# Kernel optimization log

Measured on AMD Instinct MI355X. Metric: run time of the kernel, lower is better.

## Reference

```python
import jax, jax.numpy as jnp
import numpy as np

MUL = 64                      # multiplicity of both 0e and 1o irreps
N_NODES = 10000
N_EDGES = 320000
DIM = MUL + 3 * MUL           # 64x0e + 64x1o = 256
SQ3 = float(np.sqrt(3.0))
INV_MUL = float(1.0 / np.sqrt(MUL))        # fan-in norm for irreps Linear
INV_TP = float(1.0 / np.sqrt(2 * MUL))     # fan-in norm: 2 CG paths per output irrep


def _split(f):
    # f: [E_or_N, 256] -> scalars [.,64], vectors [.,64,3]
    return f[:, :MUL], f[:, MUL:].reshape(f.shape[0], MUL, 3)


def _lin(x0, x1, w0, w1):
    # e3nn-style irreps Linear: block-diagonal per l, shared across m
    return (x0 @ w0) * INV_MUL, jnp.einsum('eum,uv->evm', x1, w1) * INV_MUL


def _fctp(x0, x1, sh1, w00, w11, w01, w10):
    # FullyConnectedTensorProduct (64x0e+64x1o) x (1x0e+1x1o) -> (64x0e+64x1o)
    # CG paths: 0e*0e->0e (identity), 1o*1o->0e (dot/sqrt3), 0e*1o->1o, 1o*0e->1o.
    # l=0 spherical harmonic == 1, so 0e SH multiplications are no-ops.
    dot = jnp.einsum('eum,em->eu', x1, sh1) / SQ3
    out0 = (x0 @ w00 + dot @ w11) * INV_TP
    out1 = (jnp.einsum('eu,uv->ev', x0, w01)[:, :, None] * sh1[:, None, :]
            + jnp.einsum('eum,uv->evm', x1, w10)) * INV_TP
    return out0, out1


def _forward(atom_feature, edge_vector, weights, edge_index):
    (ls0, ls1, ld0, ld1,
     t1_00, t1_11, t1_01, t1_10,
     t2_00, t2_11, t2_01, t2_10,
     lh0, lh1, lsc) = weights
    src, dst = edge_index[0], edge_index[1]

    # spherical harmonics of normalized edge vectors (component normalization)
    r = edge_vector / (jnp.linalg.norm(edge_vector, axis=-1, keepdims=True) + 1e-12)
    sh1 = SQ3 * r  # [E,3]; Y_0 == 1 is implicit

    x0, x1 = _split(atom_feature)
    s0, s1 = _lin(x0[src], x1[src], ls0, ls1)
    d0, d1 = _lin(x0[dst], x1[dst], ld0, ld1)  # computed but unused in the original forward

    h0, h1 = _fctp(s0, s1, sh1, t1_00, t1_11, t1_01, t1_10)
    h0, h1 = _lin(h0, h1, lh0, lh1)

    # lin_scalar: Linear(64x0e -> 64x0e+64x1o); only scalar->scalar path exists,
    # vector channels of the output are structurally zero; softmax runs over all 256.
    sc = (jax.nn.leaky_relu(h0) @ lsc) * INV_MUL
    full = jnp.concatenate([sc, jnp.zeros((sc.shape[0], 3 * MUL), sc.dtype)], axis=-1)
    act = jax.nn.softmax(full, axis=-1)  # [E,256]

    o0, o1 = _fctp(h0, h1, sh1, t2_00, t2_11, t2_01, t2_10)
    tp2_flat = jnp.concatenate([o0, o1.reshape(o1.shape[0], 3 * MUL)], axis=-1)

    msgs = act * tp2_flat  # [E,256]
    agg = jax.ops.segment_sum(msgs, dst, num_segments=atom_feature.shape[0])
    return atom_feature + agg  # residual (irreps_in == irreps_out)


_WNAMES = ['lin_src_w0', 'lin_src_w1', 'lin_dst_w0', 'lin_dst_w1',
           'tp1_w00', 'tp1_w11', 'tp1_w01', 'tp1_w10',
           'tp2_w00', 'tp2_w11', 'tp2_w01', 'tp2_w10',
           'lin_hidden_w0', 'lin_hidden_w1', 'lin_scalar_w']


def setup_inputs() -> dict:
    key = jax.random.key(0)
    ks = jax.random.split(key, 18)
    inp = {n: jax.random.normal(ks[i], (MUL, MUL), jnp.float32) for i, n in enumerate(_WNAMES)}
    inp['atom_feature'] = jax.random.normal(ks[15], (N_NODES, DIM), jnp.float32)
    inp['edge_vector'] = jax.random.normal(ks[16], (N_EDGES, 3), jnp.float32)
    inp['edge_index'] = jax.random.randint(ks[17], (2, N_EDGES), 0, N_NODES, dtype=jnp.int32)
    return inp


def reference(atom_feature, edge_vector,
              lin_src_w0, lin_src_w1, lin_dst_w0, lin_dst_w1,
              tp1_w00, tp1_w11, tp1_w01, tp1_w10,
              tp2_w00, tp2_w11, tp2_w01, tp2_w10,
              lin_hidden_w0, lin_hidden_w1, lin_scalar_w,
              edge_index):
    weights = (lin_src_w0, lin_src_w1, lin_dst_w0, lin_dst_w1,
               tp1_w00, tp1_w11, tp1_w01, tp1_w10,
               tp2_w00, tp2_w11, tp2_w01, tp2_w10,
               lin_hidden_w0, lin_hidden_w1, lin_scalar_w)
    return _forward(atom_feature, edge_vector, weights, edge_index)
```

## Files before the change

kernel.cpp:

```cpp
#include <hip/hip_runtime.h>

#define N_NODES 10000
#define N_EDGES 320000
#define DIM 256

typedef __attribute__((ext_vector_type(8))) short bf16x8;
typedef __attribute__((ext_vector_type(4))) float f32x4;

static constexpr float SQ3     = 1.7320508075688772f;
static constexpr float INV_SQ3 = 0.5773502691896258f;
static constexpr float INV_MUL = 0.125f;
static constexpr float INV_TP  = 0.08838834764831845f;

__device__ __forceinline__ unsigned short f2bf(float f) {
    unsigned b = __builtin_bit_cast(unsigned, f);
    b += 0x7FFFu + ((b >> 16) & 1u);
    return (unsigned short)(b >> 16);
}
__device__ __forceinline__ float bf2f(unsigned short h) {
    return __builtin_bit_cast(float, ((unsigned)h) << 16);
}

__device__ __forceinline__ f32x4 MFMA(bf16x8 a, bf16x8 b, f32x4 c) {
    return __builtin_amdgcn_mfma_f32_16x16x32_bf16(a, b, c, 0, 0, 0);
}

struct AF { bf16x8 hi[2], lo[2]; };

__device__ __forceinline__ void split8(const float* v, bf16x8& hi, bf16x8& lo) {
#pragma unroll
    for (int j = 0; j < 8; ++j) {
        unsigned short h = f2bf(v[j]);
        hi[j] = (short)h;
        lo[j] = (short)f2bf(v[j] - bf2f(h));
    }
}

__device__ __forceinline__ void zacc(f32x4* a) {
#pragma unroll
    for (int i = 0; i < 4; ++i) a[i] = (f32x4){0.f, 0.f, 0.f, 0.f};
}

__device__ __forceinline__ void mv_acc(const AF& a, const unsigned short* __restrict__ wm,
                                       f32x4* acc) {
    const int l = threadIdx.x & 63;
#pragma unroll
    for (int ks = 0; ks < 2; ++ks) {
#pragma unroll
        for (int nt = 0; nt < 4; ++nt) {
            bf16x8 bh = *(const bf16x8*)(wm + (ks * 4 + nt) * 512 + l * 8);
            bf16x8 bl = *(const bf16x8*)(wm + 4096 + (ks * 4 + nt) * 512 + l * 8);
            acc[nt] = MFMA(a.hi[ks], bh, acc[nt]);
            acc[nt] = MFMA(a.lo[ks], bh, acc[nt]);
            acc[nt] = MFMA(a.hi[ks], bl, acc[nt]);
        }
    }
}

__device__ __forceinline__ void store_D(float* __restrict__ buf, const f32x4* acc, float scale) {
    const int l = threadIdx.x & 63;
    const int c = l & 15, rgp = l >> 4;
#pragma unroll
    for (int nt = 0; nt < 4; ++nt)
#pragma unroll
        for (int r = 0; r < 4; ++r)
            buf[(rgp * 4 + r) * 68 + nt * 16 + c] = acc[nt][r] * scale;
}

__device__ __forceinline__ void store_D_h1(float* __restrict__ buf, const f32x4* p01,
                                           const float shDm[4], const f32x4* acc) {
    const int l = threadIdx.x & 63;
    const int c = l & 15, rgp = l >> 4;
#pragma unroll
    for (int nt = 0; nt < 4; ++nt)
#pragma unroll
        for (int r = 0; r < 4; ++r)
            buf[(rgp * 4 + r) * 68 + nt * 16 + c] =
                (p01[nt][r] * shDm[r] + acc[nt][r]) * INV_TP;
}

__device__ __forceinline__ void read_row8(const float* __restrict__ buf, int ks, float* v) {
    const int l = threadIdx.x & 63;
    const float* p = buf + (l & 15) * 68 + (l >> 4) * 8 + ks * 32;
    f32x4 x = *(const f32x4*)(p);
    f32x4 y = *(const f32x4*)(p + 4);
    v[0] = x[0]; v[1] = x[1]; v[2] = x[2]; v[3] = x[3];
    v[4] = y[0]; v[5] = y[1]; v[6] = y[2]; v[7] = y[3];
}

__device__ __forceinline__ void build_A(const float* __restrict__ buf, AF& a) {
#pragma unroll
    for (int ks = 0; ks < 2; ++ks) {
        float v[8];
        read_row8(buf, ks, v);
        split8(v, a.hi[ks], a.lo[ks]);
    }
}

__device__ __forceinline__ void build_A_dot(const float* __restrict__ buf, AF& a, float shm,
                                            float dv[2][8]) {
#pragma unroll
    for (int ks = 0; ks < 2; ++ks) {
        float v[8];
        read_row8(buf, ks, v);
#pragma unroll
        for (int j = 0; j < 8; ++j) dv[ks][j] = fmaf(v[j], shm, dv[ks][j]);
        split8(v, a.hi[ks], a.lo[ks]);
    }
}

__device__ __forceinline__ void build_A_leaky(const float* __restrict__ buf, AF& a, AF& alr) {
#pragma unroll
    for (int ks = 0; ks < 2; ++ks) {
        float v[8];
        read_row8(buf, ks, v);
        split8(v, a.hi[ks], a.lo[ks]);
        float w[8];
#pragma unroll
        for (int j = 0; j < 8; ++j) w[j] = v[j] > 0.f ? v[j] : 0.01f * v[j];
        split8(w, alr.hi[ks], alr.lo[ks]);
    }
}

__global__ __launch_bounds__(256) void init_out_kernel(const float* __restrict__ af,
                                                       float* __restrict__ out) {
    int i = blockIdx.x * blockDim.x + threadIdx.x;
    reinterpret_cast<float4*>(out)[i] = reinterpret_cast<const float4*>(af)[i];
}

__global__ __launch_bounds__(256) void prep_w(
    const float* a0, const float* a1, const float* a2, const float* a3,
    const float* a4, const float* a5, const float* a6, const float* a7,
    const float* a8, const float* a9, const float* a10, const float* a11,
    const float* a12, unsigned short* __restrict__ o)
{
    const float* mats[13] = {a0,a1,a2,a3,a4,a5,a6,a7,a8,a9,a10,a11,a12};
    const float* W = mats[blockIdx.x];
    unsigned short* dst = o + blockIdx.x * 8192;
    for (int t = threadIdx.x; t < 4096; t += 256) {
        int u = t >> 6, v = t & 63;
        float val = W[t];
        unsigned short hi = f2bf(val);
        unsigned short lo = f2bf(val - bf2f(hi));
        int ks = u >> 5, g = (u >> 3) & 3, j = u & 7;
        int base = ((ks * 4 + (v >> 4)) * 64 + ((v & 15) + 16 * g)) * 8 + j;
        dst[base] = hi;
        dst[4096 + base] = lo;
    }
}

__global__ __launch_bounds__(256, 2) void edge_kernel(
    const float* __restrict__ af, const float* __restrict__ ev,
    const int* __restrict__ ei, const unsigned short* __restrict__ wb,
    float* __restrict__ out)
{
    __shared__ float lds[4][4][16 * 68];
    const int l  = threadIdx.x & 63;
    const int wv = threadIdx.x >> 6;
    const int rg = l >> 4;
    const int e0 = (blockIdx.x * 4 + wv) * 16;
    float* B0 = lds[wv][0];
    float* B1 = lds[wv][1];
    float* B2 = lds[wv][2];
    float* B3 = lds[wv][3];
    float* Bm[3] = {B1, B2, B3};

    float shA[3];
    {
        int e = e0 + (l & 15);
        float x = ev[3*e], y = ev[3*e+1], z = ev[3*e+2];
        float s = SQ3 / (sqrtf(x*x + y*y + z*z) + 1e-12f);
        shA[0] = x*s; shA[1] = y*s; shA[2] = z*s;
    }
    float shD[4][3]; int dstD[4];
#pragma unroll
    for (int r = 0; r < 4; ++r) {
        int e = e0 + rg * 4 + r;
        float x = ev[3*e], y = ev[3*e+1], z = ev[3*e+2];
        float s = SQ3 / (sqrtf(x*x + y*y + z*z) + 1e-12f);
        shD[r][0] = x*s; shD[r][1] = y*s; shD[r][2] = z*s;
        dstD[r] = ei[N_EDGES + e];
    }

    AF x0a, x1a[3];
    {
        const int node = ei[e0 + (l & 15)];
        const float* rp = af + (long)node * DIM;
#pragma unroll
        for (int ks = 0; ks < 2; ++ks) {
            const int u0 = rg * 8 + ks * 32;
            f32x4 xa = *(const f32x4*)(rp + u0);
            f32x4 xb = *(const f32x4*)(rp + u0 + 4);
            float v[8] = {xa[0],xa[1],xa[2],xa[3],xb[0],xb[1],xb[2],xb[3]};
            split8(v, x0a.hi[ks], x0a.lo[ks]);
            f32x4 sp[6];
#pragma unroll
            for (int q = 0; q < 6; ++q) sp[q] = *(const f32x4*)(rp + 64 + 3 * u0 + 4 * q);
#pragma unroll
            for (int m = 0; m < 3; ++m) {
                float w[8];
#pragma unroll
                for (int j = 0; j < 8; ++j) { int idx = 3 * j + m; w[j] = sp[idx >> 2][idx & 3]; }
                split8(w, x1a[m].hi[ks], x1a[m].lo[ks]);
            }
        }
    }

    f32x4 acc[4];

#pragma unroll
    for (int m = 0; m < 3; ++m) {
        zacc(acc); mv_acc(x1a[m], wb + 1 * 8192, acc);
        store_D(Bm[m], acc, INV_MUL);
    }
    zacc(acc); mv_acc(x0a, wb + 0 * 8192, acc);
    store_D(B0, acc, INV_MUL);
    asm volatile("s_waitcnt lgkmcnt(0)" ::: "memory");

    AF s0a, s1a[3], dota;
    build_A(B0, s0a);
    {
        float dv[2][8] = {};
#pragma unroll
        for (int m = 0; m < 3; ++m) build_A_dot(Bm[m], s1a[m], shA[m], dv);
        float d0[8], d1[8];
#pragma unroll
        for (int j = 0; j < 8; ++j) { d0[j] = dv[0][j] * INV_SQ3; d1[j] = dv[1][j] * INV_SQ3; }
        split8(d0, dota.hi[0], dota.lo[0]);
        split8(d1, dota.hi[1], dota.lo[1]);
    }

    zacc(acc); mv_acc(s0a, wb + 2 * 8192, acc); mv_acc(dota, wb + 3 * 8192, acc);
    store_D(B0, acc, INV_TP);
    f32x4 p01[4];
    zacc(p01); mv_acc(s0a, wb + 4 * 8192, p01);
#pragma unroll
    for (int m = 0; m < 3; ++m) {
        zacc(acc); mv_acc(s1a[m], wb + 5 * 8192, acc);
        float shm[4] = {shD[0][m], shD[1][m], shD[2][m], shD[3][m]};
        store_D_h1(Bm[m], p01, shm, acc);
    }
    asm volatile("s_waitcnt lgkmcnt(0)" ::: "memory");

    AF h0a, h1a[3];
    build_A(B0, h0a);
#pragma unroll
    for (int m = 0; m < 3; ++m) build_A(Bm[m], h1a[m]);
    zacc(acc); mv_acc(h0a, wb + 6 * 8192, acc);
    store_D(B0, acc, INV_MUL);
#pragma unroll
    for (int m = 0; m < 3; ++m) {
        zacc(acc); mv_acc(h1a[m], wb + 7 * 8192, acc);
        store_D(Bm[m], acc, INV_MUL);
    }
    asm volatile("s_waitcnt lgkmcnt(0)" ::: "memory");

    AF g0a, lra, g1a[3], dot2a;
    build_A_leaky(B0, g0a, lra);
    {
        float dv[2][8] = {};
#pragma unroll
        for (int m = 0; m < 3; ++m) build_A_dot(Bm[m], g1a[m], shA[m], dv);
        float d0[8], d1[8];
#pragma unroll
        for (int j = 0; j < 8; ++j) { d0[j] = dv[0][j] * INV_SQ3; d1[j] = dv[1][j] * INV_SQ3; }
        split8(d0, dot2a.hi[0], dot2a.lo[0]);
        split8(d1, dot2a.hi[1], dot2a.lo[1]);
    }

    f32x4 sc[4];
    zacc(sc); mv_acc(lra, wb + 8 * 8192, sc);
    float act1r[4];
    {
#pragma unroll
        for (int nt = 0; nt < 4; ++nt) sc[nt] *= INV_MUL;
#pragma unroll
        for (int r = 0; r < 4; ++r) {
            float mx = fmaxf(fmaxf(sc[0][r], sc[1][r]), fmaxf(sc[2][r], sc[3][r]));
#pragma unroll
            for (int w = 1; w <= 8; w <<= 1) mx = fmaxf(mx, __shfl_xor(mx, w, 64));
            mx = fmaxf(mx, 0.f);
            float s_ = 0.f;
#pragma unroll
            for (int nt = 0; nt < 4; ++nt) { float p = __expf(sc[nt][r] - mx); sc[nt][r] = p; s_ += p; }
#pragma unroll
            for (int w = 1; w <= 8; w <<= 1) s_ += __shfl_xor(s_, w, 64);
            float ez = __expf(-mx);
            float invZ = 1.0f / (s_ + 192.f * ez);
#pragma unroll
            for (int nt = 0; nt < 4; ++nt) sc[nt][r] *= invZ;
            act1r[r] = ez * invZ;
        }
    }

    f32x4 o0[4];
    zacc(o0); mv_acc(g0a, wb + 9 * 8192, o0); mv_acc(dot2a, wb + 10 * 8192, o0);
    f32x4 qD[4];
    zacc(qD); mv_acc(g0a, wb + 11 * 8192, qD);

#pragma unroll
    for (int nt = 0; nt < 4; ++nt)
#pragma unroll
        for (int r = 0; r < 4; ++r)
            atomicAdd(out + (long)dstD[r] * DIM + nt * 16 + (l & 15),
                      sc[nt][r] * o0[nt][r] * INV_TP);

#pragma unroll
    for (int m = 0; m < 3; ++m) {
        zacc(acc); mv_acc(g1a[m], wb + 12 * 8192, acc);
#pragma unroll
        for (int nt = 0; nt < 4; ++nt)
#pragma unroll
            for (int r = 0; r < 4; ++r) {
                float val = (qD[nt][r] * shD[r][m] + acc[nt][r]) * INV_TP * act1r[r];
                atomicAdd(out + (long)dstD[r] * DIM + 64 + 3 * (nt * 16 + (l & 15)) + m, val);
            }
    }
}

extern "C" void kernel_launch(void* const* d_in, const int* in_sizes, int n_in,
                              void* d_out, int out_size, void* d_ws, size_t ws_size,
                              hipStream_t stream) {
    const float* ls0  = (const float*)d_in[0];
    const float* ls1  = (const float*)d_in[1];
    const float* t100 = (const float*)d_in[4];
    const float* t111 = (const float*)d_in[5];
    const float* t101 = (const float*)d_in[6];
    const float* t110 = (const float*)d_in[7];
    const float* t200 = (const float*)d_in[8];
    const float* t211 = (const float*)d_in[9];
    const float* t201 = (const float*)d_in[10];
    const float* t210 = (const float*)d_in[11];
    const float* lh0  = (const float*)d_in[12];
    const float* lh1  = (const float*)d_in[13];
    const float* lsc  = (const float*)d_in[14];
    const float* af   = (const float*)d_in[15];
    const float* ev   = (const float*)d_in[16];
    const int*   ei   = (const int*)d_in[17];
    float* out = (float*)d_out;
    unsigned short* wbuf = (unsigned short*)d_ws;

    hipLaunchKernelGGL(prep_w, dim3(13), dim3(256), 0, stream,
                       ls0, ls1, t100, t111, t101, t110, lh0, lh1, lsc,
                       t200, t211, t201, t210, wbuf);

    hipLaunchKernelGGL(init_out_kernel, dim3(N_NODES * DIM / 4 / 256), dim3(256), 0, stream,
                       af, out);

    hipLaunchKernelGGL(edge_kernel, dim3(N_EDGES / 64), dim3(256), 0, stream,
                       af, ev, ei, wbuf, out);
}
```

Measured before the change: 785.3 us.

## Halve per-wave LDS staging buffers and raise occupancy to four blocks

Each wave's LDS staging shrinks from four 16x68 buffers to two, and the matmul stages are reordered to ping-pong between them. Each build reads a buffer right after its store, with an explicit LDS wait. This cuts LDS per block in half, and launch_bounds is raised from 2 to 4 blocks per CU to use that for more occupancy. The cost is more frequent lgkmcnt waits, which serialise store and read phases, and a tighter register budget that may cause spills.

New measurement: 863.0 us. 9.9% more time.

```diff
diff --git a/kernel.cpp b/kernel.cpp
--- a/kernel.cpp
+++ b/kernel.cpp
@@ -149,21 +149,20 @@
     }
 }
 
-__global__ __launch_bounds__(256, 2) void edge_kernel(
+#define WAIT_LDS asm volatile("s_waitcnt lgkmcnt(0)" ::: "memory")
+
+__global__ __launch_bounds__(256, 4) void edge_kernel(
     const float* __restrict__ af, const float* __restrict__ ev,
     const int* __restrict__ ei, const unsigned short* __restrict__ wb,
     float* __restrict__ out)
 {
-    __shared__ float lds[4][4][16 * 68];
+    __shared__ float lds[4][2][16 * 68];
     const int l  = threadIdx.x & 63;
     const int wv = threadIdx.x >> 6;
     const int rg = l >> 4;
     const int e0 = (blockIdx.x * 4 + wv) * 16;
     float* B0 = lds[wv][0];
     float* B1 = lds[wv][1];
-    float* B2 = lds[wv][2];
-    float* B3 = lds[wv][3];
-    float* Bm[3] = {B1, B2, B3};
 
     float shA[3];
     {
@@ -207,22 +206,18 @@
     }
 
     f32x4 acc[4];
-
-#pragma unroll
-    for (int m = 0; m < 3; ++m) {
-        zacc(acc); mv_acc(x1a[m], wb + 1 * 8192, acc);
-        store_D(Bm[m], acc, INV_MUL);
-    }
-    zacc(acc); mv_acc(x0a, wb + 0 * 8192, acc);
-    store_D(B0, acc, INV_MUL);
-    asm volatile("s_waitcnt lgkmcnt(0)" ::: "memory");
-
     AF s0a, s1a[3], dota;
-    build_A(B0, s0a);
+
+    zacc(acc); mv_acc(x1a[0], wb + 1 * 8192, acc); store_D(B0, acc, INV_MUL);
+    zacc(acc); mv_acc(x1a[1], wb + 1 * 8192, acc); store_D(B1, acc, INV_MUL);
     {
         float dv[2][8] = {};
-#pragma unroll
-        for (int m = 0; m < 3; ++m) build_A_dot(Bm[m], s1a[m], shA[m], dv);
+        WAIT_LDS; build_A_dot(B0, s1a[0], shA[0], dv);
+        zacc(acc); mv_acc(x1a[2], wb + 1 * 8192, acc); store_D(B0, acc, INV_MUL);
+        WAIT_LDS; build_A_dot(B1, s1a[1], shA[1], dv);
+        zacc(acc); mv_acc(x0a, wb + 0 * 8192, acc); store_D(B1, acc, INV_MUL);
+        WAIT_LDS; build_A_dot(B0, s1a[2], shA[2], dv);
+        build_A(B1, s0a);
         float d0[8], d1[8];
 #pragma unroll
         for (int j = 0; j < 8; ++j) { d0[j] = dv[0][j] * INV_SQ3; d1[j] = dv[1][j] * INV_SQ3; }
@@ -230,37 +225,39 @@
         split8(d1, dota.hi[1], dota.lo[1]);
     }
 
+    AF h0a, h1a[3];
     zacc(acc); mv_acc(s0a, wb + 2 * 8192, acc); mv_acc(dota, wb + 3 * 8192, acc);
     store_D(B0, acc, INV_TP);
     f32x4 p01[4];
     zacc(p01); mv_acc(s0a, wb + 4 * 8192, p01);
-#pragma unroll
-    for (int m = 0; m < 3; ++m) {
-        zacc(acc); mv_acc(s1a[m], wb + 5 * 8192, acc);
-        float shm[4] = {shD[0][m], shD[1][m], shD[2][m], shD[3][m]};
-        store_D_h1(Bm[m], p01, shm, acc);
-    }
-    asm volatile("s_waitcnt lgkmcnt(0)" ::: "memory");
-
-    AF h0a, h1a[3];
-    build_A(B0, h0a);
-#pragma unroll
-    for (int m = 0; m < 3; ++m) build_A(Bm[m], h1a[m]);
+    zacc(acc); mv_acc(s1a[0], wb + 5 * 8192, acc);
+    { float shm[4] = {shD[0][0], shD[1][0], shD[2][0], shD[3][0]};
+      store_D_h1(B1, p01, shm, acc); }
+    WAIT_LDS; build_A(B0, h0a);
+    zacc(acc); mv_acc(s1a[1], wb + 5 * 8192, acc);
+    { float shm[4] = {shD[0][1], shD[1][1], shD[2][1], shD[3][1]};
+      store_D_h1(B0, p01, shm, acc); }
+    WAIT_LDS; build_A(B1, h1a[0]);
+    zacc(acc); mv_acc(s1a[2], wb + 5 * 8192, acc);
+    { float shm[4] = {shD[0][2], shD[1][2], shD[2][2], shD[3][2]};
+      store_D_h1(B1, p01, shm, acc); }
+    WAIT_LDS; build_A(B0, h1a[1]);
     zacc(acc); mv_acc(h0a, wb + 6 * 8192, acc);
     store_D(B0, acc, INV_MUL);
-#pragma unroll
-    for (int m = 0; m < 3; ++m) {
-        zacc(acc); mv_acc(h1a[m], wb + 7 * 8192, acc);
-        store_D(Bm[m], acc, INV_MUL);
-    }
-    asm volatile("s_waitcnt lgkmcnt(0)" ::: "memory");
-
+    WAIT_LDS; build_A(B1, h1a[2]);
+    zacc(acc); mv_acc(h1a[0], wb + 7 * 8192, acc);
+    store_D(B1, acc, INV_MUL);
     AF g0a, lra, g1a[3], dot2a;
-    build_A_leaky(B0, g0a, lra);
+    WAIT_LDS; build_A_leaky(B0, g0a, lra);
+    zacc(acc); mv_acc(h1a[1], wb + 7 * 8192, acc);
+    store_D(B0, acc, INV_MUL);
     {
         float dv[2][8] = {};
-#pragma unroll
-        for (int m = 0; m < 3; ++m) build_A_dot(Bm[m], g1a[m], shA[m], dv);
+        WAIT_LDS; build_A_dot(B1, g1a[0], shA[0], dv);
+        zacc(acc); mv_acc(h1a[2], wb + 7 * 8192, acc);
+        store_D(B1, acc, INV_MUL);
+        WAIT_LDS; build_A_dot(B0, g1a[1], shA[1], dv);
+        build_A_dot(B1, g1a[2], shA[2], dv);
         float d0[8], d1[8];
 #pragma unroll
         for (int j = 0; j < 8; ++j) { d0[j] = dv[0][j] * INV_SQ3; d1[j] = dv[1][j] * INV_SQ3; }
```

## Restructure edge kernel to two LDS buffers and streamed fragments for occupancy

Applied to the files above, without the earlier changes.

Reorders the edge kernel so each vector component's fragments are built, consumed and discarded one at a time, ping-ponging between two LDS buffers per wave instead of four. Spherical-harmonic and destination values are recomputed or reloaded where needed rather than held in registers. It also targets three waves per EU instead of launch_bounds(256,2), aiming to cut register and LDS pressure and raise occupancy to hide atomic and gather latency. The cost is extra reloads of edge vectors and tighter ordering that depends on per-wave LDS reuse with no explicit waitcnt.

New measurement: 967.8 us. 1.23x slower.

```diff
diff --git a/kernel.cpp b/kernel.cpp
--- a/kernel.cpp
+++ b/kernel.cpp
@@ -68,15 +68,18 @@
 }
 
 __device__ __forceinline__ void store_D_h1(float* __restrict__ buf, const f32x4* p01,
-                                           const float shDm[4], const f32x4* acc) {
+                                           const f32x4* acc, const float* __restrict__ ev,
+                                           int e0, int m, const float invn[4]) {
     const int l = threadIdx.x & 63;
     const int c = l & 15, rgp = l >> 4;
 #pragma unroll
-    for (int nt = 0; nt < 4; ++nt)
-#pragma unroll
-        for (int r = 0; r < 4; ++r)
+    for (int r = 0; r < 4; ++r) {
+        const float shm = SQ3 * ev[3 * (e0 + rgp * 4 + r) + m] * invn[r];
+#pragma unroll
+        for (int nt = 0; nt < 4; ++nt)
             buf[(rgp * 4 + r) * 68 + nt * 16 + c] =
-                (p01[nt][r] * shDm[r] + acc[nt][r]) * INV_TP;
+                (p01[nt][r] * shm + acc[nt][r]) * INV_TP;
+    }
 }
 
 __device__ __forceinline__ void read_row8(const float* __restrict__ buf, int ks, float* v) {
@@ -119,6 +122,31 @@
 #pragma unroll
         for (int j = 0; j < 8; ++j) w[j] = v[j] > 0.f ? v[j] : 0.01f * v[j];
         split8(w, alr.hi[ks], alr.lo[ks]);
+    }
+}
+
+__device__ __forceinline__ void build_x0(const float* __restrict__ rp, int rg, AF& a) {
+#pragma unroll
+    for (int ks = 0; ks < 2; ++ks) {
+        const int u0 = rg * 8 + ks * 32;
+        f32x4 xa = *(const f32x4*)(rp + u0);
+        f32x4 xb = *(const f32x4*)(rp + u0 + 4);
+        float v[8] = {xa[0], xa[1], xa[2], xa[3], xb[0], xb[1], xb[2], xb[3]};
+        split8(v, a.hi[ks], a.lo[ks]);
+    }
+}
+__device__ __forceinline__ void build_x1(const float* __restrict__ rp, int m, int rg, AF& a) {
+#pragma unroll
+    for (int ks = 0; ks < 2; ++ks) {
+        const int u0 = rg * 8 + ks * 32;
+        const float* q = rp + 64 + 3 * u0;
+        f32x4 sp[6];
+#pragma unroll
+        for (int qq = 0; qq < 6; ++qq) sp[qq] = *(const f32x4*)(q + 4 * qq);
+        float w[8];
+#pragma unroll
+        for (int j = 0; j < 8; ++j) { int idx = 3 * j + m; w[j] = sp[idx >> 2][idx & 3]; }
+        split8(w, a.hi[ks], a.lo[ks]);
     }
 }
 
@@ -149,80 +177,51 @@
     }
 }
 
-__global__ __launch_bounds__(256, 2) void edge_kernel(
+__global__ __attribute__((amdgpu_waves_per_eu(3, 3))) __launch_bounds__(256)
+void edge_kernel(
     const float* __restrict__ af, const float* __restrict__ ev,
     const int* __restrict__ ei, const unsigned short* __restrict__ wb,
     float* __restrict__ out)
 {
-    __shared__ float lds[4][4][16 * 68];
+    __shared__ float lds[4][2][16 * 68];
     const int l  = threadIdx.x & 63;
     const int wv = threadIdx.x >> 6;
     const int rg = l >> 4;
+    const int c  = l & 15;
     const int e0 = (blockIdx.x * 4 + wv) * 16;
     float* B0 = lds[wv][0];
     float* B1 = lds[wv][1];
-    float* B2 = lds[wv][2];
-    float* B3 = lds[wv][3];
-    float* Bm[3] = {B1, B2, B3};
 
     float shA[3];
     {
-        int e = e0 + (l & 15);
+        int e = e0 + c;
         float x = ev[3*e], y = ev[3*e+1], z = ev[3*e+2];
         float s = SQ3 / (sqrtf(x*x + y*y + z*z) + 1e-12f);
         shA[0] = x*s; shA[1] = y*s; shA[2] = z*s;
     }
-    float shD[4][3]; int dstD[4];
+    float invn[4];
 #pragma unroll
     for (int r = 0; r < 4; ++r) {
         int e = e0 + rg * 4 + r;
         float x = ev[3*e], y = ev[3*e+1], z = ev[3*e+2];
-        float s = SQ3 / (sqrtf(x*x + y*y + z*z) + 1e-12f);
-        shD[r][0] = x*s; shD[r][1] = y*s; shD[r][2] = z*s;
-        dstD[r] = ei[N_EDGES + e];
-    }
-
-    AF x0a, x1a[3];
-    {
-        const int node = ei[e0 + (l & 15)];
-        const float* rp = af + (long)node * DIM;
-#pragma unroll
-        for (int ks = 0; ks < 2; ++ks) {
-            const int u0 = rg * 8 + ks * 32;
-            f32x4 xa = *(const f32x4*)(rp + u0);
-            f32x4 xb = *(const f32x4*)(rp + u0 + 4);
-            float v[8] = {xa[0],xa[1],xa[2],xa[3],xb[0],xb[1],xb[2],xb[3]};
-            split8(v, x0a.hi[ks], x0a.lo[ks]);
-            f32x4 sp[6];
-#pragma unroll
-            for (int q = 0; q < 6; ++q) sp[q] = *(const f32x4*)(rp + 64 + 3 * u0 + 4 * q);
-#pragma unroll
-            for (int m = 0; m < 3; ++m) {
-                float w[8];
-#pragma unroll
-                for (int j = 0; j < 8; ++j) { int idx = 3 * j + m; w[j] = sp[idx >> 2][idx & 3]; }
-                split8(w, x1a[m].hi[ks], x1a[m].lo[ks]);
-            }
-        }
-    }
+        invn[r] = 1.0f / (sqrtf(x*x + y*y + z*z) + 1e-12f);
+    }
+    const float* rp = af + (long)ei[e0 + c] * DIM;
 
     f32x4 acc[4];
-
-#pragma unroll
-    for (int m = 0; m < 3; ++m) {
-        zacc(acc); mv_acc(x1a[m], wb + 1 * 8192, acc);
-        store_D(Bm[m], acc, INV_MUL);
-    }
-    zacc(acc); mv_acc(x0a, wb + 0 * 8192, acc);
-    store_D(B0, acc, INV_MUL);
-    asm volatile("s_waitcnt lgkmcnt(0)" ::: "memory");
-
-    AF s0a, s1a[3], dota;
-    build_A(B0, s0a);
+    AF t;
+    AF s1a0, s1a1, s1a2, s0a, dota;
+
+    build_x1(rp, 0, rg, t); zacc(acc); mv_acc(t, wb + 1*8192, acc); store_D(B0, acc, INV_MUL);
+    build_x1(rp, 1, rg, t); zacc(acc); mv_acc(t, wb + 1*8192, acc); store_D(B1, acc, INV_MUL);
     {
         float dv[2][8] = {};
-#pragma unroll
-        for (int m = 0; m < 3; ++m) build_A_dot(Bm[m], s1a[m], shA[m], dv);
+        build_A_dot(B0, s1a0, shA[0], dv);
+        build_x1(rp, 2, rg, t); zacc(acc); mv_acc(t, wb + 1*8192, acc); store_D(B0, acc, INV_MUL);
+        build_A_dot(B1, s1a1, shA[1], dv);
+        build_x0(rp, rg, t);    zacc(acc); mv_acc(t, wb + 0*8192, acc); store_D(B1, acc, INV_MUL);
+        build_A_dot(B0, s1a2, shA[2], dv);
+        build_A(B1, s0a);
         float d0[8], d1[8];
 #pragma unroll
         for (int j = 0; j < 8; ++j) { d0[j] = dv[0][j] * INV_SQ3; d1[j] = dv[1][j] * INV_SQ3; }
@@ -230,46 +229,35 @@
         split8(d1, dota.hi[1], dota.lo[1]);
     }
 
-    zacc(acc); mv_acc(s0a, wb + 2 * 8192, acc); mv_acc(dota, wb + 3 * 8192, acc);
+    zacc(acc); mv_acc(s0a, wb + 2*8192, acc); mv_acc(dota, wb + 3*8192, acc);
     store_D(B0, acc, INV_TP);
     f32x4 p01[4];
-    zacc(p01); mv_acc(s0a, wb + 4 * 8192, p01);
-#pragma unroll
-    for (int m = 0; m < 3; ++m) {
-        zacc(acc); mv_acc(s1a[m], wb + 5 * 8192, acc);
-        float shm[4] = {shD[0][m], shD[1][m], shD[2][m], shD[3][m]};
-        store_D_h1(Bm[m], p01, shm, acc);
-    }
-    asm volatile("s_waitcnt lgkmcnt(0)" ::: "memory");
-
-    AF h0a, h1a[3];
-    build_A(B0, h0a);
-#pragma unroll
-    for (int m = 0; m < 3; ++m) build_A(Bm[m], h1a[m]);
-    zacc(acc); mv_acc(h0a, wb + 6 * 8192, acc);
+    zacc(p01); mv_acc(s0a, wb + 4*8192, p01);
+    zacc(acc); mv_acc(s1a0, wb + 5*8192, acc);
+    store_D_h1(B1, p01, acc, ev, e0, 0, invn);
+    AF h0a; build_A(B0, h0a);
+    zacc(acc); mv_acc(s1a1, wb + 5*8192, acc);
+    store_D_h1(B0, p01, acc, ev, e0, 1, invn);
+    AF h1a0; build_A(B1, h1a0);
+    zacc(acc); mv_acc(s1a2, wb + 5*8192, acc);
+    store_D_h1(B1, p01, acc, ev, e0, 2, invn);
+
+    zacc(acc); mv_acc(h0a, wb + 6*8192, acc);
+    AF h1a1; build_A(B0, h1a1);
     store_D(B0, acc, INV_MUL);
-#pragma unroll
-    for (int m = 0; m < 3; ++m) {
-        zacc(acc); mv_acc(h1a[m], wb + 7 * 8192, acc);
-        store_D(Bm[m], acc, INV_MUL);
-    }
-    asm volatile("s_waitcnt lgkmcnt(0)" ::: "memory");
-
-    AF g0a, lra, g1a[3], dot2a;
-    build_A_leaky(B0, g0a, lra);
-    {
-        float dv[2][8] = {};
-#pragma unroll
-        for (int m = 0; m < 3; ++m) build_A_dot(Bm[m], g1a[m], shA[m], dv);
-        float d0[8], d1[8];
-#pragma unroll
-        for (int j = 0; j < 8; ++j) { d0[j] = dv[0][j] * INV_SQ3; d1[j] = dv[1][j] * INV_SQ3; }
-        split8(d0, dot2a.hi[0], dot2a.lo[0]);
-        split8(d1, dot2a.hi[1], dot2a.lo[1]);
-    }
+    zacc(acc); mv_acc(h1a0, wb + 7*8192, acc);
+    AF h1a2; build_A(B1, h1a2);
+    store_D(B1, acc, INV_MUL);
+    zacc(acc); mv_acc(h1a1, wb + 7*8192, acc);
+    AF g0a, lra; build_A_leaky(B0, g0a, lra);
+    store_D(B0, acc, INV_MUL);
+    zacc(acc); mv_acc(h1a2, wb + 7*8192, acc);
+    AF g1a; float dv2[2][8] = {};
+    build_A_dot(B1, g1a, shA[0], dv2);
+    store_D(B1, acc, INV_MUL);
 
     f32x4 sc[4];
-    zacc(sc); mv_acc(lra, wb + 8 * 8192, sc);
+    zacc(sc); mv_acc(lra, wb + 8*8192, sc);
     float act1r[4];
     {
 #pragma unroll
@@ -293,29 +281,56 @@
         }
     }
 
-    f32x4 o0[4];
-    zacc(o0); mv_acc(g0a, wb + 9 * 8192, o0); mv_acc(dot2a, wb + 10 * 8192, o0);
-    f32x4 qD[4];
-    zacc(qD); mv_acc(g0a, wb + 11 * 8192, qD);
-
+    f32x4 qD[4]; zacc(qD); mv_acc(g0a, wb + 11*8192, qD);
+    f32x4 o0[4]; zacc(o0); mv_acc(g0a, wb + 9*8192, o0);
+    int dstD[4];
+#pragma unroll
+    for (int r = 0; r < 4; ++r) dstD[r] = ei[N_EDGES + e0 + rg * 4 + r];
+
+    zacc(acc); mv_acc(g1a, wb + 12*8192, acc);
+#pragma unroll
+    for (int r = 0; r < 4; ++r) {
+        const float shm = SQ3 * ev[3 * (e0 + rg * 4 + r) + 0] * invn[r];
+#pragma unroll
+        for (int nt = 0; nt < 4; ++nt)
+            atomicAdd(out + (long)dstD[r] * DIM + 64 + 3 * (nt * 16 + c) + 0,
+                      (qD[nt][r] * shm + acc[nt][r]) * INV_TP * act1r[r]);
+    }
+    build_A_dot(B0, g1a, shA[1], dv2);
+    zacc(acc); mv_acc(g1a, wb + 12*8192, acc);
+#pragma unroll
+    for (int r = 0; r < 4; ++r) {
+        const float shm = SQ3 * ev[3 * (e0 + rg * 4 + r) + 1] * invn[r];
+#pragma unroll
+        for (int nt = 0; nt < 4; ++nt)
+            atomicAdd(out + (long)dstD[r] * DIM + 64 + 3 * (nt * 16 + c) + 1,
+                      (qD[nt][r] * shm + acc[nt][r]) * INV_TP * act1r[r]);
+    }
+    build_A_dot(B1, g1a, shA[2], dv2);
+    zacc(acc); mv_acc(g1a, wb + 12*8192, acc);
+#pragma unroll
+    for (int r = 0; r < 4; ++r) {
+        const float shm = SQ3 * ev[3 * (e0 + rg * 4 + r) + 2] * invn[r];
+#pragma unroll
+        for (int nt = 0; nt < 4; ++nt)
+            atomicAdd(out + (long)dstD[r] * DIM + 64 + 3 * (nt * 16 + c) + 2,
+                      (qD[nt][r] * shm + acc[nt][r]) * INV_TP * act1r[r]);
+    }
+    {
+        AF dot2a;
+        float d0[8], d1[8];
+#pragma unroll
+        for (int j = 0; j < 8; ++j) { d0[j] = dv2[0][j] * INV_SQ3; d1[j] = dv2[1][j] * INV_SQ3; }
+        split8(d0, dot2a.hi[0], dot2a.lo[0]);
+        split8(d1, dot2a.hi[1], dot2a.lo[1]);
+        mv_acc(dot2a, wb + 10*8192, o0);
+    }
 #pragma unroll
     for (int nt = 0; nt < 4; ++nt)
 #pragma unroll
         for (int r = 0; r < 4; ++r)
-            atomicAdd(out + (long)dstD[r] * DIM + nt * 16 + (l & 15),
+            atomicAdd(out + (long)dstD[r] * DIM + nt * 16 + c,
                       sc[nt][r] * o0[nt][r] * INV_TP);
-
-#pragma unroll
-    for (int m = 0; m < 3; ++m) {
-        zacc(acc); mv_acc(g1a[m], wb + 12 * 8192, acc);
-#pragma unroll
-        for (int nt = 0; nt < 4; ++nt)
-#pragma unroll
-            for (int r = 0; r < 4; ++r) {
-                float val = (qD[nt][r] * shD[r][m] + acc[nt][r]) * INV_TP * act1r[r];
-                atomicAdd(out + (long)dstD[r] * DIM + 64 + 3 * (nt * 16 + (l & 15)) + m, val);
-            }
-    }
 }
 
 extern "C" void kernel_launch(void* const* d_in, const int* in_sizes, int n_in,
```
